# Performance work log

Measured on AMD Instinct MI355X. Metric: run time of the kernel, lower is better.

Reference implementation:

```python
import jax, jax.numpy as jnp
import numpy as np

NUM_MEM, MEM_DIM, INP_DIM, N = 4096, 512, 1024, 32768

def setup_inputs() -> dict:
    key = jax.random.key(0)
    ks = jax.random.split(key, 6)
    s = 1.0 / np.sqrt(MEM_DIM)
    return {
        "k": jax.random.normal(ks[0], (N, INP_DIM), dtype=jnp.float32),
        "mem": jax.random.normal(ks[1], (NUM_MEM, MEM_DIM), dtype=jnp.float32),
        "fk_w": jax.random.uniform(ks[2], (INP_DIM, MEM_DIM), jnp.float32, -s, s),
        "fk_b": jax.random.uniform(ks[3], (INP_DIM,), jnp.float32, -s, s),
        "fv_w": jax.random.uniform(ks[4], (INP_DIM, MEM_DIM), jnp.float32, -s, s),
        "fv_b": jax.random.uniform(ks[5], (INP_DIM,), jnp.float32, -s, s),
    }

def reference(k, mem, fk_w, fk_b, fv_w, fv_b):
    # key/value derivation from the memory bank: [num_mem, inp_dim]
    key = jax.nn.softmax(mem @ fk_w.T + fk_b, axis=-1)
    val = jax.nn.relu(mem @ fv_w.T + fv_b)
    # attention read: [n, num_mem]
    att = jax.nn.softmax(k @ key.T, axis=-1)
    # output: [n, inp_dim]
    return att @ val
```

## Files before the change

kernel.cpp:

```cpp
#include <hip/hip_runtime.h>
#include <stdint.h>

typedef unsigned short u16;
typedef short s16x8 __attribute__((ext_vector_type(8)));
typedef float f32x4 __attribute__((ext_vector_type(4)));

__device__ __forceinline__ u16 f2bf(float f) {
    union { float f; uint32_t i; } v; v.f = f;
    return (u16)((v.i + 0x7FFFu + ((v.i >> 16) & 1u)) >> 16);
}

__global__ void __launch_bounds__(256) cvt_f32_bf16(
    const float* __restrict__ src, u16* __restrict__ dst, int n4)
{
    int i = blockIdx.x * 256 + threadIdx.x;
    if (i >= n4) return;
    float4 f = ((const float4*)src)[i];
    ushort4 o;
    o.x = f2bf(f.x); o.y = f2bf(f.y); o.z = f2bf(f.z); o.w = f2bf(f.w);
    ((ushort4*)dst)[i] = o;
}

#define ASYNC_LD16(gp, lp)                                                       \
    __builtin_amdgcn_global_load_lds(                                            \
        (const __attribute__((address_space(1))) uint32_t*)(gp),                 \
        (__attribute__((address_space(3))) uint32_t*)(lp), 16, 0, 0)

template <int MODE>
__global__ void __launch_bounds__(256) gemm_bt(
    const u16* __restrict__ A, const u16* __restrict__ B, int K, int N,
    u16* __restrict__ C, float* __restrict__ Cf,
    const float* __restrict__ bias,
    const float* __restrict__ sv, float* __restrict__ sum_out)
{
    __shared__ __align__(16) u16 As[128 * 32];
    __shared__ __align__(16) u16 Bs[128 * 32];

    const int tid  = threadIdx.x;
    const int lane = tid & 63;
    const int wave = tid >> 6;
    const int wx = wave & 1, wy = wave >> 1;
    const int lr = lane & 15, lq = lane >> 4;
    const int m0 = blockIdx.y * 128, n0 = blockIdx.x * 128;

    f32x4 acc[4][4] = {};

    const int srow = tid >> 2;
    const int scol = (tid & 3) * 8;
    const u16* gA = A + (size_t)(m0 + srow) * K + scol;
    const u16* gB = B + (size_t)(n0 + srow) * K + scol;
    const size_t rstep = (size_t)64 * K;
    u16* lA0 = &As[wave * 512];
    u16* lA1 = &As[2048 + wave * 512];
    u16* lB0 = &Bs[wave * 512];
    u16* lB1 = &Bs[2048 + wave * 512];

    const u16* pa = &As[(wy * 64 + lr) * 32 + lq * 8];
    const u16* pb = &Bs[(wx * 64 + lr) * 32 + lq * 8];

    for (int k0 = 0; k0 < K; k0 += 32) {
        ASYNC_LD16(gA + k0, lA0);
        ASYNC_LD16(gA + k0 + rstep, lA1);
        ASYNC_LD16(gB + k0, lB0);
        ASYNC_LD16(gB + k0 + rstep, lB1);
        __syncthreads();
        s16x8 af[4], bfr[4];
#pragma unroll
        for (int i = 0; i < 4; ++i) {
            af[i]  = *(const s16x8*)(pa + i * 512);
            bfr[i] = *(const s16x8*)(pb + i * 512);
        }
#pragma unroll
        for (int mi = 0; mi < 4; ++mi)
#pragma unroll
            for (int ni = 0; ni < 4; ++ni)
                acc[mi][ni] = __builtin_amdgcn_mfma_f32_16x16x32_bf16(
                    af[mi], bfr[ni], acc[mi][ni], 0, 0, 0);
        __syncthreads();
    }

    const int rowB = m0 + wy * 64 + lq * 4;
    const int colB = n0 + wx * 64 + lr;

    if constexpr (MODE == 0) {
        float bcol[4];
#pragma unroll
        for (int ni = 0; ni < 4; ++ni) bcol[ni] = bias[colB + ni * 16];
#pragma unroll
        for (int mi = 0; mi < 4; ++mi)
#pragma unroll
            for (int r = 0; r < 4; ++r) {
                const int gm = rowB + mi * 16 + r;
                float s = 0.f;
#pragma unroll
                for (int ni = 0; ni < 4; ++ni) {
                    float e = __expf(acc[mi][ni][r] + bcol[ni]);
                    C[(size_t)gm * N + (colB + ni * 16)] = f2bf(e);
                    s += e;
                }
                s += __shfl_xor(s, 1);
                s += __shfl_xor(s, 2);
                s += __shfl_xor(s, 4);
                s += __shfl_xor(s, 8);
                if (lr == 0) atomicAdd(&sum_out[gm], s);
            }
    } else {
#pragma unroll
        for (int mi = 0; mi < 4; ++mi)
#pragma unroll
            for (int r = 0; r < 4; ++r) {
                const int gm = rowB + mi * 16 + r;
                const float b = bias[gm];
#pragma unroll
                for (int ni = 0; ni < 4; ++ni) {
                    float c = acc[mi][ni][r] + b;
                    C[(size_t)gm * N + (colB + ni * 16)] = f2bf(c > 0.f ? c : 0.f);
                }
            }
    }
}

template <int MODE>
__global__ void __launch_bounds__(512, 2) gemm256_bt(
    const u16* __restrict__ A, const u16* __restrict__ B, int K, int N,
    u16* __restrict__ C, float* __restrict__ Cf,
    const float* __restrict__ sv, float* __restrict__ sum_out, int nbx)
{
    __shared__ __align__(16) u16 lds[4 * 16384];

    const int tid  = threadIdx.x;
    const int lane = tid & 63;
    const int wave = tid >> 6;
    const int wr = wave >> 2;
    const int wc = wave & 3;
    const int fr = lane & 15;
    const int lq = lane >> 4;

    const int nwg = gridDim.x;
    const int swz = ((int)blockIdx.x & 7) * (nwg >> 3) + ((int)blockIdx.x >> 3);
    const int bx = swz % nbx, by = swz / nbx;
    const int m0 = by * 256, n0 = bx * 256;

    const int r0 = tid >> 2;
    const int r1 = r0 + 128;
    const int gch = (tid & 3) ^ ((r0 >> 1) & 3);
    const u16* gA0 = A + (size_t)(m0 + r0) * K + gch * 8;
    const u16* gA1 = A + (size_t)(m0 + r1) * K + gch * 8;
    const u16* gB0 = B + (size_t)(n0 + r0) * K + gch * 8;
    const u16* gB1 = B + (size_t)(n0 + r1) * K + gch * 8;

#define STG_A(bf_, kt_) do {                                                  \
        ASYNC_LD16(gA0 + (kt_) * 32, lds + (bf_) * 16384 + wave * 512);       \
        ASYNC_LD16(gA1 + (kt_) * 32, lds + (bf_) * 16384 + 4096 + wave * 512);\
    } while (0)
#define STG_B(bf_, kt_) do {                                                  \
        ASYNC_LD16(gB0 + (kt_) * 32, lds + (bf_) * 16384 + 8192 + wave * 512);\
        ASYNC_LD16(gB1 + (kt_) * 32, lds + (bf_) * 16384 + 12288 + wave * 512);\
    } while (0)

    const int rch = lq ^ ((fr >> 1) & 3);
    const int offA0 = (wr * 128 + fr) * 32 + rch * 8;
    const int offB0 = (wc * 64 + fr) * 32 + rch * 8;

    f32x4 acc[8][4] = {};
    const int NT = K >> 5;

    STG_A(0, 0); STG_B(0, 0);
    STG_A(1, 1); STG_B(1, 1);
    STG_A(2, 2); STG_B(2, 2);
    asm volatile("s_waitcnt vmcnt(8)" ::: "memory");
    __builtin_amdgcn_s_barrier();

    for (int c = 0; c < NT; ++c) {
        const u16* sA = lds + (c & 3) * 16384;
        const u16* sB = sA + 8192;
        if (c + 3 < NT) { STG_A((c + 3) & 3, c + 3); STG_B((c + 3) & 3, c + 3); }
        s16x8 a[8], b[4];
#pragma unroll
        for (int i = 0; i < 8; ++i) a[i] = *(const s16x8*)(sA + offA0 + i * 512);
#pragma unroll
        for (int i = 0; i < 4; ++i) b[i] = *(const s16x8*)(sB + offB0 + i * 512);
        __builtin_amdgcn_s_setprio(1);
#pragma unroll
        for (int mi = 0; mi < 8; ++mi)
#pragma unroll
            for (int ni = 0; ni < 4; ++ni)
                acc[mi][ni] = __builtin_amdgcn_mfma_f32_16x16x32_bf16(
                    a[mi], b[ni], acc[mi][ni], 0, 0, 0);
        __builtin_amdgcn_s_setprio(0);
        asm volatile("s_waitcnt vmcnt(8)" ::: "memory");
        __builtin_amdgcn_s_barrier();
    }

    const int rowB = m0 + wr * 128 + lq * 4;
    const int colB = n0 + wc * 64 + fr;

    if constexpr (MODE == 2) {
        float inv[4];
#pragma unroll
        for (int ni = 0; ni < 4; ++ni) inv[ni] = 1.0f / sv[colB + ni * 16];
#pragma unroll
        for (int mi = 0; mi < 8; ++mi)
#pragma unroll
            for (int r = 0; r < 4; ++r) {
                const int gm = rowB + mi * 16 + r;
                float s = 0.f;
#pragma unroll
                for (int ni = 0; ni < 4; ++ni) {
                    float e = __expf(acc[mi][ni][r] * inv[ni]);
                    C[(size_t)gm * N + (colB + ni * 16)] = f2bf(e);
                    s += e;
                }
                s += __shfl_xor(s, 1);
                s += __shfl_xor(s, 2);
                s += __shfl_xor(s, 4);
                s += __shfl_xor(s, 8);
                if (fr == 0) atomicAdd(&sum_out[gm], s);
            }
    } else {
#pragma unroll
        for (int mi = 0; mi < 8; ++mi)
#pragma unroll
            for (int r = 0; r < 4; ++r) {
                const int gm = rowB + mi * 16 + r;
                const float invr = 1.0f / sv[gm];
#pragma unroll
                for (int ni = 0; ni < 4; ++ni)
                    Cf[(size_t)gm * N + (colB + ni * 16)] = acc[mi][ni][r] * invr;
            }
    }
#undef STG_A
#undef STG_B
}

extern "C" void kernel_launch(void* const* d_in, const int* in_sizes, int n_in,
                              void* d_out, int out_size, void* d_ws, size_t ws_size,
                              hipStream_t stream)
{
    (void)in_sizes; (void)n_in; (void)out_size;
    const float* kin = (const float*)d_in[0];
    const float* mem = (const float*)d_in[1];
    const float* fkw = (const float*)d_in[2];
    const float* fkb = (const float*)d_in[3];
    const float* fvw = (const float*)d_in[4];
    const float* fvb = (const float*)d_in[5];
    float* out = (float*)d_out;

    const int NM = 4096, MD = 512, ID = 1024, NQ = 32768;

    u16* kbf   = (u16*)d_ws;
    u16* membf = kbf   + (size_t)NQ * ID;
    u16* fkwbf = membf + (size_t)NM * MD;
    u16* fvwbf = fkwbf + (size_t)ID * MD;
    u16* expK  = fvwbf + (size_t)ID * MD;
    u16* valT  = expK  + (size_t)NM * ID;
    u16* P     = valT  + (size_t)ID * NM;
    float* rsK = (float*)(P + (size_t)NQ * NM);
    float* rs2 = rsK + NM;
    const size_t needed = (size_t)((char*)(rs2 + NQ) - (char*)d_ws);
    if (ws_size < needed) return;

    hipMemsetAsync(rsK, 0, (size_t)(NM + NQ) * sizeof(float), stream);

    cvt_f32_bf16<<<(NQ * ID / 4 + 255) / 256, 256, 0, stream>>>(kin, kbf, NQ * ID / 4);
    cvt_f32_bf16<<<(NM * MD / 4 + 255) / 256, 256, 0, stream>>>(mem, membf, NM * MD / 4);
    cvt_f32_bf16<<<(ID * MD / 4 + 255) / 256, 256, 0, stream>>>(fkw, fkwbf, ID * MD / 4);
    cvt_f32_bf16<<<(ID * MD / 4 + 255) / 256, 256, 0, stream>>>(fvw, fvwbf, ID * MD / 4);

    gemm_bt<0><<<dim3(ID / 128, NM / 128), 256, 0, stream>>>(
        membf, fkwbf, MD, ID, expK, nullptr, fkb, nullptr, rsK);
    gemm_bt<1><<<dim3(NM / 128, ID / 128), 256, 0, stream>>>(
        fvwbf, membf, MD, NM, valT, nullptr, fvb, nullptr, nullptr);
    gemm256_bt<2><<<(NQ / 256) * (NM / 256), 512, 0, stream>>>(
        kbf, expK, ID, NM, P, nullptr, rsK, rs2, NM / 256);
    gemm256_bt<3><<<(NQ / 256) * (ID / 256), 512, 0, stream>>>(
        P, valT, NM, ID, nullptr, out, rs2, nullptr, ID / 256);
}
```

Before: 920.3 us.

## Software-pipeline LDS fragment loads with MFMA in the bf16 GEMM main loop

The GEMM main loop is unrolled by two and each K-step is split into two MFMA halves. B and upper-A fragments are read first. The next stage's lower-A fragments are prefetched from LDS between the halves, and the async global->LDS issue for A and B is interleaved with compute. The wait count drops from vmcnt(8) to vmcnt(4), keeping more stages resident before each barrier, and sched_barriers pin the instruction order. This aims to hide LDS read latency behind MFMA work, at the cost of more registers for the extra fragment buffers and an assumption that the number of K tiles is even.

```diff
diff --git a/kernel.cpp b/kernel.cpp
--- a/kernel.cpp
+++ b/kernel.cpp
@@ -159,8 +159,8 @@
     } while (0)
 
     const int rch = lq ^ ((fr >> 1) & 3);
-    const int offA0 = (wr * 128 + fr) * 32 + rch * 8;
-    const int offB0 = (wc * 64 + fr) * 32 + rch * 8;
+    const int offA = (wr * 128 + fr) * 32 + rch * 8;
+    const int offB = (wc * 64 + fr) * 32 + rch * 8 + 8192;
 
     f32x4 acc[8][4] = {};
     const int NT = K >> 5;
@@ -168,29 +168,51 @@
     STG_A(0, 0); STG_B(0, 0);
     STG_A(1, 1); STG_B(1, 1);
     STG_A(2, 2); STG_B(2, 2);
-    asm volatile("s_waitcnt vmcnt(8)" ::: "memory");
+    asm volatile("s_waitcnt vmcnt(4)" ::: "memory");
     __builtin_amdgcn_s_barrier();
-
-    for (int c = 0; c < NT; ++c) {
-        const u16* sA = lds + (c & 3) * 16384;
-        const u16* sB = sA + 8192;
-        if (c + 3 < NT) { STG_A((c + 3) & 3, c + 3); STG_B((c + 3) & 3, c + 3); }
-        s16x8 a[8], b[4];
-#pragma unroll
-        for (int i = 0; i < 8; ++i) a[i] = *(const s16x8*)(sA + offA0 + i * 512);
-#pragma unroll
-        for (int i = 0; i < 4; ++i) b[i] = *(const s16x8*)(sB + offB0 + i * 512);
-        __builtin_amdgcn_s_setprio(1);
-#pragma unroll
-        for (int mi = 0; mi < 8; ++mi)
-#pragma unroll
-            for (int ni = 0; ni < 4; ++ni)
-                acc[mi][ni] = __builtin_amdgcn_mfma_f32_16x16x32_bf16(
-                    a[mi], b[ni], acc[mi][ni], 0, 0, 0);
-        __builtin_amdgcn_s_setprio(0);
-        asm volatile("s_waitcnt vmcnt(8)" ::: "memory");
-        __builtin_amdgcn_s_barrier();
-    }
+    __builtin_amdgcn_sched_barrier(0);
+
+    s16x8 aLo0[4], aLo1[4], aHi[4], bv[4];
+#pragma unroll
+    for (int i = 0; i < 4; ++i)
+        aLo0[i] = *(const s16x8*)(lds + offA + i * 512);
+
+#define ITER(c_, AL, ALN)                                                     \
+    {                                                                         \
+        const u16* sCur = lds + ((c_) & 3) * 16384;                           \
+        const u16* sNxt = lds + (((c_) + 1) & 3) * 16384;                     \
+        _Pragma("unroll") for (int i = 0; i < 4; ++i)                         \
+            bv[i] = *(const s16x8*)(sCur + offB + i * 512);                   \
+        _Pragma("unroll") for (int i = 0; i < 4; ++i)                         \
+            aHi[i] = *(const s16x8*)(sCur + offA + (i + 4) * 512);            \
+        if ((c_) + 3 < NT) STG_A(((c_) + 3) & 3, (c_) + 3);                   \
+        __builtin_amdgcn_s_setprio(1);                                        \
+        _Pragma("unroll") for (int mi = 0; mi < 4; ++mi)                      \
+            _Pragma("unroll") for (int ni = 0; ni < 4; ++ni)                  \
+                acc[mi][ni] = __builtin_amdgcn_mfma_f32_16x16x32_bf16(        \
+                    AL[mi], bv[ni], acc[mi][ni], 0, 0, 0);                    \
+        __builtin_amdgcn_s_setprio(0);                                        \
+        _Pragma("unroll") for (int i = 0; i < 4; ++i)                         \
+            ALN[i] = *(const s16x8*)(sNxt + offA + i * 512);                  \
+        if ((c_) + 3 < NT) STG_B(((c_) + 3) & 3, (c_) + 3);                   \
+        __builtin_amdgcn_s_setprio(1);                                        \
+        _Pragma("unroll") for (int mi = 0; mi < 4; ++mi)                      \
+            _Pragma("unroll") for (int ni = 0; ni < 4; ++ni)                  \
+                acc[mi + 4][ni] = __builtin_amdgcn_mfma_f32_16x16x32_bf16(    \
+                    aHi[mi], bv[ni], acc[mi + 4][ni], 0, 0, 0);               \
+        __builtin_amdgcn_s_setprio(0);                                        \
+        asm volatile("s_waitcnt vmcnt(4)" ::: "memory");                      \
+        __builtin_amdgcn_s_barrier();                                         \
+        __builtin_amdgcn_sched_barrier(0);                                    \
+    }
+
+    for (int c = 0; c < NT; c += 2) {
+        ITER(c,     aLo0, aLo1);
+        ITER(c + 1, aLo1, aLo0);
+    }
+#undef ITER
+#undef STG_A
+#undef STG_B
 
     const int rowB = m0 + wr * 128 + lq * 4;
     const int colB = n0 + wc * 64 + fr;
@@ -229,8 +251,6 @@
                     Cf[(size_t)gm * N + (colB + ni * 16)] = acc[mi][ni][r] * invr;
             }
     }
-#undef STG_A
-#undef STG_B
 }
 
 extern "C" void kernel_launch(void* const* d_in, const int* in_sizes, int n_in,
```

Result: no change. 902.9 us (-1.9%).

## Shrink big GEMM tiles to 128x128 with 4 waves and triple buffering

Applied to the files above, without the earlier changes.

Replaces the 256x256, 8-wave, 4-stage GEMM used for the two large products with a 128x128, 4-wave kernel that has a 3-stage LDS ring and a prefetch depth of 2. The goal is higher occupancy (3 blocks per CU, smaller LDS footprint) and more blocks to balance across CUs. In exchange, each loaded element is reused less, so global/L2 traffic per FLOP rises and the async prefetch depth is lower, which may expose more memory latency.

```diff
diff --git a/kernel.cpp b/kernel.cpp
--- a/kernel.cpp
+++ b/kernel.cpp
@@ -121,78 +121,76 @@
 }
 
 template <int MODE>
-__global__ void __launch_bounds__(512, 2) gemm256_bt(
+__global__ void __launch_bounds__(256, 3) gemm128p_bt(
     const u16* __restrict__ A, const u16* __restrict__ B, int K, int N,
     u16* __restrict__ C, float* __restrict__ Cf,
     const float* __restrict__ sv, float* __restrict__ sum_out, int nbx)
 {
-    __shared__ __align__(16) u16 lds[4 * 16384];
+    __shared__ __align__(16) u16 lds[3 * 8192];
 
     const int tid  = threadIdx.x;
     const int lane = tid & 63;
     const int wave = tid >> 6;
-    const int wr = wave >> 2;
-    const int wc = wave & 3;
+    const int wr = wave >> 1;
+    const int wc = wave & 1;
     const int fr = lane & 15;
     const int lq = lane >> 4;
 
     const int nwg = gridDim.x;
     const int swz = ((int)blockIdx.x & 7) * (nwg >> 3) + ((int)blockIdx.x >> 3);
     const int bx = swz % nbx, by = swz / nbx;
-    const int m0 = by * 256, n0 = bx * 256;
-
-    const int r0 = tid >> 2;
-    const int r1 = r0 + 128;
+    const int m0 = by * 128, n0 = bx * 128;
+
+    const int r0  = tid >> 2;
     const int gch = (tid & 3) ^ ((r0 >> 1) & 3);
     const u16* gA0 = A + (size_t)(m0 + r0) * K + gch * 8;
-    const u16* gA1 = A + (size_t)(m0 + r1) * K + gch * 8;
+    const u16* gA1 = A + (size_t)(m0 + r0 + 64) * K + gch * 8;
     const u16* gB0 = B + (size_t)(n0 + r0) * K + gch * 8;
-    const u16* gB1 = B + (size_t)(n0 + r1) * K + gch * 8;
-
-#define STG_A(bf_, kt_) do {                                                  \
-        ASYNC_LD16(gA0 + (kt_) * 32, lds + (bf_) * 16384 + wave * 512);       \
-        ASYNC_LD16(gA1 + (kt_) * 32, lds + (bf_) * 16384 + 4096 + wave * 512);\
+    const u16* gB1 = B + (size_t)(n0 + r0 + 64) * K + gch * 8;
+
+#define STG(bf_, kt_) do {                                                    \
+        ASYNC_LD16(gA0 + (kt_) * 32, lds + (bf_) * 8192 + wave * 512);        \
+        ASYNC_LD16(gA1 + (kt_) * 32, lds + (bf_) * 8192 + 2048 + wave * 512); \
+        ASYNC_LD16(gB0 + (kt_) * 32, lds + (bf_) * 8192 + 4096 + wave * 512); \
+        ASYNC_LD16(gB1 + (kt_) * 32, lds + (bf_) * 8192 + 6144 + wave * 512); \
     } while (0)
-#define STG_B(bf_, kt_) do {                                                  \
-        ASYNC_LD16(gB0 + (kt_) * 32, lds + (bf_) * 16384 + 8192 + wave * 512);\
-        ASYNC_LD16(gB1 + (kt_) * 32, lds + (bf_) * 16384 + 12288 + wave * 512);\
-    } while (0)
-
-    const int rch = lq ^ ((fr >> 1) & 3);
-    const int offA0 = (wr * 128 + fr) * 32 + rch * 8;
-    const int offB0 = (wc * 64 + fr) * 32 + rch * 8;
-
-    f32x4 acc[8][4] = {};
+
+    const int rch  = lq ^ ((fr >> 1) & 3);
+    const int offA = (wr * 64 + fr) * 32 + rch * 8;
+    const int offB = 4096 + (wc * 64 + fr) * 32 + rch * 8;
+
+    f32x4 acc[4][4] = {};
     const int NT = K >> 5;
 
-    STG_A(0, 0); STG_B(0, 0);
-    STG_A(1, 1); STG_B(1, 1);
-    STG_A(2, 2); STG_B(2, 2);
-    asm volatile("s_waitcnt vmcnt(8)" ::: "memory");
+    STG(0, 0);
+    STG(1, 1);
+    asm volatile("s_waitcnt vmcnt(4)" ::: "memory");
     __builtin_amdgcn_s_barrier();
 
+    int cur = 0, stg = 2;
     for (int c = 0; c < NT; ++c) {
-        const u16* sA = lds + (c & 3) * 16384;
-        const u16* sB = sA + 8192;
-        if (c + 3 < NT) { STG_A((c + 3) & 3, c + 3); STG_B((c + 3) & 3, c + 3); }
-        s16x8 a[8], b[4];
-#pragma unroll
-        for (int i = 0; i < 8; ++i) a[i] = *(const s16x8*)(sA + offA0 + i * 512);
-#pragma unroll
-        for (int i = 0; i < 4; ++i) b[i] = *(const s16x8*)(sB + offB0 + i * 512);
+        const u16* s = lds + cur * 8192;
+        if (c + 2 < NT) STG(stg, c + 2);
+        s16x8 a[4], b[4];
+#pragma unroll
+        for (int i = 0; i < 4; ++i) a[i] = *(const s16x8*)(s + offA + i * 512);
+#pragma unroll
+        for (int i = 0; i < 4; ++i) b[i] = *(const s16x8*)(s + offB + i * 512);
         __builtin_amdgcn_s_setprio(1);
 #pragma unroll
-        for (int mi = 0; mi < 8; ++mi)
+        for (int mi = 0; mi < 4; ++mi)
 #pragma unroll
             for (int ni = 0; ni < 4; ++ni)
                 acc[mi][ni] = __builtin_amdgcn_mfma_f32_16x16x32_bf16(
                     a[mi], b[ni], acc[mi][ni], 0, 0, 0);
         __builtin_amdgcn_s_setprio(0);
-        asm volatile("s_waitcnt vmcnt(8)" ::: "memory");
+        asm volatile("s_waitcnt vmcnt(4)" ::: "memory");
         __builtin_amdgcn_s_barrier();
-    }
-
-    const int rowB = m0 + wr * 128 + lq * 4;
+        cur = (cur == 2) ? 0 : cur + 1;
+        stg = (stg == 2) ? 0 : stg + 1;
+    }
+
+    const int rowB = m0 + wr * 64 + lq * 4;
     const int colB = n0 + wc * 64 + fr;
 
     if constexpr (MODE == 2) {
@@ -200,7 +198,7 @@
 #pragma unroll
         for (int ni = 0; ni < 4; ++ni) inv[ni] = 1.0f / sv[colB + ni * 16];
 #pragma unroll
-        for (int mi = 0; mi < 8; ++mi)
+        for (int mi = 0; mi < 4; ++mi)
 #pragma unroll
             for (int r = 0; r < 4; ++r) {
                 const int gm = rowB + mi * 16 + r;
@@ -219,7 +217,7 @@
             }
     } else {
 #pragma unroll
-        for (int mi = 0; mi < 8; ++mi)
+        for (int mi = 0; mi < 4; ++mi)
 #pragma unroll
             for (int r = 0; r < 4; ++r) {
                 const int gm = rowB + mi * 16 + r;
@@ -229,8 +227,7 @@
                     Cf[(size_t)gm * N + (colB + ni * 16)] = acc[mi][ni][r] * invr;
             }
     }
-#undef STG_A
-#undef STG_B
+#undef STG
 }
 
 extern "C" void kernel_launch(void* const* d_in, const int* in_sizes, int n_in,
@@ -271,8 +268,8 @@
         membf, fkwbf, MD, ID, expK, nullptr, fkb, nullptr, rsK);
     gemm_bt<1><<<dim3(NM / 128, ID / 128), 256, 0, stream>>>(
         fvwbf, membf, MD, NM, valT, nullptr, fvb, nullptr, nullptr);
-    gemm256_bt<2><<<(NQ / 256) * (NM / 256), 512, 0, stream>>>(
-        kbf, expK, ID, NM, P, nullptr, rsK, rs2, NM / 256);
-    gemm256_bt<3><<<(NQ / 256) * (ID / 256), 512, 0, stream>>>(
-        P, valT, NM, ID, nullptr, out, rs2, nullptr, ID / 256);
-}
+    gemm128p_bt<2><<<(NQ / 128) * (NM / 128), 256, 0, stream>>>(
+        kbf, expK, ID, NM, P, nullptr, rsK, rs2, NM / 128);
+    gemm128p_bt<3><<<(NQ / 128) * (ID / 128), 256, 0, stream>>>(
+        P, valT, NM, ID, nullptr, out, rs2, nullptr, ID / 128);
+}
```

New measurement: 1.016 ms. +10.4%, slower.
